# Optimization experiments

Measured on AMD Instinct MI355X. Metric: run time of the kernel, lower is better.

Reference implementation:

```python
import jax, jax.numpy as jnp
import numpy as np

B, S, D = 8, 4096, 1024
H = 16
HD = D // H          # 64
FF = 128             # FeedForward default intermediate_size
EPS = 1e-6           # flax RMSNorm default


def _rmsnorm(x, g):
    return x * jax.lax.rsqrt(jnp.mean(x * x, axis=-1, keepdims=True) + EPS) * g


def setup_inputs() -> dict:
    key = jax.random.key(0)
    ks = jax.random.split(key, 12)
    s = 0.02
    return {
        "x": jax.random.normal(ks[0], (B, S, D), jnp.float32),
        "attention_mask": jnp.ones((B, HD), jnp.int32),
        # per-head QKV projections stacked over heads: [H, D, HD]
        "Wq": jax.random.normal(ks[1], (H, D, HD), jnp.float32) * s,
        "bq": jnp.zeros((H, HD), jnp.float32),
        "Wk": jax.random.normal(ks[2], (H, D, HD), jnp.float32) * s,
        "bk": jnp.zeros((H, HD), jnp.float32),
        "Wv": jax.random.normal(ks[3], (H, D, HD), jnp.float32) * s,
        "bv": jnp.zeros((H, HD), jnp.float32),
        "Wo": jax.random.normal(ks[4], (D, D), jnp.float32) * s,
        "bo": jnp.zeros((D,), jnp.float32),
        "W1": jax.random.normal(ks[5], (D, FF), jnp.float32) * s,
        "b1": jnp.zeros((FF,), jnp.float32),
        "W2": jax.random.normal(ks[6], (FF, D), jnp.float32) * s,
        "b2": jnp.zeros((D,), jnp.float32),
        "g1": jnp.ones((D,), jnp.float32),
        "g2": jnp.ones((D,), jnp.float32),
    }


def reference(x, attention_mask, Wq, bq, Wk, bk, Wv, bv, Wo, bo, W1, b1, W2, b2, g1, g2):
    # per-head projections, vectorized over heads: [B, H, S, HD]
    q = jnp.einsum('bsd,hde->bhse', x, Wq) + bq[:, None, :]
    k = jnp.einsum('bsd,hde->bhse', x, Wk) + bk[:, None, :]
    v = jnp.einsum('bsd,hde->bhse', x, Wv) + bv[:, None, :]
    # scores = k^T @ q -> [B, H, HD(kfeat), HD(qfeat)]  (feature-feature attention)
    scores = jnp.einsum('bhsk,bhsq->bhkq', k, q)
    # tiled mask: each row of [HD, HD] equals mask -> masks along last (q-feature) axis
    m = attention_mask[:, None, None, :]  # [B,1,1,HD]
    scores = jnp.where(m == 0, -jnp.inf, scores)
    w = jax.nn.softmax(scores / jnp.sqrt(jnp.float32(HD)), axis=-2)
    # out = v @ w -> [B, H, S, HD]
    attn = jnp.einsum('bhsk,bhkq->bhsq', v, w)
    attn = attn.transpose(0, 2, 1, 3).reshape(B, S, D)  # concat heads
    # output projection + residual + RMSNorm
    h = x + attn @ Wo + bo
    h = _rmsnorm(h, g1)
    # tanh FFN + residual + RMSNorm
    ff = jnp.tanh(h @ W1 + b1) @ W2 + b2
    out = _rmsnorm(h + ff, g2)
    return out
```

## Files before the change

### kernel.cpp

```cpp
#include <hip/hip_runtime.h>
#include <math.h>

typedef __attribute__((ext_vector_type(4))) float f32x4;
typedef __attribute__((ext_vector_type(8))) short short8;
typedef __attribute__((ext_vector_type(4))) short short4v;

__device__ __forceinline__ float b2f(unsigned short u) {
  unsigned int x = ((unsigned int)u) << 16;
  return __builtin_bit_cast(float, x);
}
__device__ __forceinline__ unsigned short f2b(float f) {
  unsigned int x = __builtin_bit_cast(unsigned int, f);
  x += 0x7fffu + ((x >> 16) & 1u);
  return (unsigned short)(x >> 16);
}

__device__ __forceinline__ void gload16(const unsigned short* g, unsigned short* l) {
  __builtin_amdgcn_global_load_lds(
      (__attribute__((address_space(1))) void*)(unsigned long long)(const void*)g,
      (__attribute__((address_space(3))) void*)l, 16, 0, 0);
}

#define BARR  { __builtin_amdgcn_sched_barrier(0); __builtin_amdgcn_s_barrier(); __builtin_amdgcn_sched_barrier(0); }
#define LBARR { __builtin_amdgcn_sched_barrier(0); asm volatile("s_waitcnt lgkmcnt(0)" ::: "memory"); __builtin_amdgcn_s_barrier(); __builtin_amdgcn_sched_barrier(0); }
#define VMW(n) { __builtin_amdgcn_sched_barrier(0); asm volatile("s_waitcnt vmcnt(" #n ")" ::: "memory"); __builtin_amdgcn_sched_barrier(0); }

__global__ __launch_bounds__(256) void prep_kernel(
    const float* __restrict__ x, unsigned short* __restrict__ xb,
    const float* __restrict__ Wq, const float* __restrict__ Wk,
    const float* __restrict__ Wv, const float* __restrict__ Wo,
    const float* __restrict__ W1, const float* __restrict__ W2,
    const float* __restrict__ bq, const float* __restrict__ bk, const float* __restrict__ bv,
    const float* __restrict__ g1,
    unsigned short* __restrict__ BqkT, unsigned short* __restrict__ WoT,
    unsigned short* __restrict__ W1T, unsigned short* __restrict__ W2T,
    unsigned short* __restrict__ WvR,
    float* __restrict__ bqkv) {
  __shared__ float tile[64][65];
  int nb = blockIdx.x, t = threadIdx.x;
  if (nb < 16384) {
    long i = (long)nb * 256 + t;
    f32x4 a = ((const f32x4*)x)[i * 2];
    f32x4 b = ((const f32x4*)x)[i * 2 + 1];
    short8 o;
#pragma unroll
    for (int j = 0; j < 4; ++j) { o[j] = (short)f2b(a[j]); o[4 + j] = (short)f2b(b[j]); }
    ((short8*)xb)[i] = o;
    return;
  }
  int n0 = nb - 16384;
  if (n0 == 1088) {
#pragma unroll
    for (int it = 0; it < 12; ++it) {
      int idx = it * 256 + t;
      float v = (idx < 1024) ? bq[idx] : (idx < 2048 ? bk[idx - 1024] : bv[idx - 2048]);
      bqkv[idx] = v;
    }
    return;
  }
  if (n0 >= 832) {
    int rem = n0 - 832, h = rem >> 4, dc = rem & 15;
    int r = t >> 2, c0 = (t & 3) * 16;
    const float* s = Wv + ((long)h * 1024 + dc * 64 + r) * 64 + c0;
    unsigned short* d = WvR + (long)(dc * 64 + r) * 1024 + h * 64 + c0;
#pragma unroll
    for (int j4 = 0; j4 < 4; ++j4) {
      f32x4 v = *(const f32x4*)(s + j4 * 4);
      short4v o;
#pragma unroll
      for (int j = 0; j < 4; ++j) o[j] = (short)f2b(v[j]);
      *(short4v*)(d + j4 * 4) = o;
    }
    return;
  }
  const float* src; unsigned short* dst; int sld, dld;
  bool foldg = false; int dbase = 0;
  if (n0 < 512) {
    int w = n0 >> 8, rem = n0 & 255, h = rem >> 4, dc = rem & 15;
    const float* W = (w == 0) ? Wq : Wk;
    src = W + ((long)h * 1024 + dc * 64) * 64;                 sld = 64;
    dst = BqkT + (long)(w * 1024 + h * 64) * 1024 + dc * 64;   dld = 1024;
  } else if (n0 < 768) {
    int rem = n0 - 512, dr = rem >> 4, jc = rem & 15;
    src = Wo + (long)dr * 64 * 1024 + jc * 64;                 sld = 1024;
    dst = WoT + (long)jc * 64 * 1024 + dr * 64;                dld = 1024;
  } else if (n0 < 800) {
    int rem = n0 - 768, dr = rem >> 1, fc = rem & 1;
    src = W1 + (long)dr * 64 * 128 + fc * 64;                  sld = 128;
    dst = W1T + (long)fc * 64 * 1024 + dr * 64;                dld = 1024;
    foldg = true; dbase = dr * 64;
  } else {
    int rem = n0 - 800, fr = rem >> 4, jc = rem & 15;
    src = W2 + (long)fr * 64 * 1024 + jc * 64;                 sld = 1024;
    dst = W2T + (long)jc * 64 * 128 + fr * 64;                 dld = 128;
  }
  int r = t >> 2, c0 = (t & 3) * 16;
#pragma unroll
  for (int j4 = 0; j4 < 4; ++j4) {
    f32x4 v = *(const f32x4*)(src + (long)r * sld + c0 + j4 * 4);
    tile[c0 + j4 * 4 + 0][r] = v[0];
    tile[c0 + j4 * 4 + 1][r] = v[1];
    tile[c0 + j4 * 4 + 2][r] = v[2];
    tile[c0 + j4 * 4 + 3][r] = v[3];
  }
  __syncthreads();
  short8 o0, o1;
#pragma unroll
  for (int j = 0; j < 8; ++j) {
    float v0 = tile[r][c0 + j], v1 = tile[r][c0 + 8 + j];
    if (foldg) { v0 *= g1[dbase + c0 + j]; v1 *= g1[dbase + c0 + 8 + j]; }
    o0[j] = (short)f2b(v0);
    o1[j] = (short)f2b(v1);
  }
  *(short8*)(dst + (long)r * dld + c0) = o0;
  *(short8*)(dst + (long)r * dld + c0 + 8) = o1;
}

__device__ __forceinline__ void rdA2(short8 (&dst)[4][2], const char* paK0,
                                     const char* paK1, int off) {
#pragma unroll
  for (int fr = 0; fr < 4; ++fr) {
    dst[fr][0] = *(const short8*)(paK0 + off + fr * 2048);
    dst[fr][1] = *(const short8*)(paK1 + off + fr * 2048);
  }
}
__device__ __forceinline__ void rdB2(short8 (&dst)[2][2], const char* pbK0,
                                     const char* pbK1, int off) {
#pragma unroll
  for (int gr = 0; gr < 2; ++gr) {
    dst[gr][0] = *(const short8*)(pbK0 + off + gr * 2048);
    dst[gr][1] = *(const short8*)(pbK1 + off + gr * 2048);
  }
}
template <int BPH>
__device__ __forceinline__ void mfmaq_f(const short8 (&afr)[4][2], const short8 (&bf)[2][2],
                                        f32x4 (*ac)[4]) {
  __builtin_amdgcn_s_setprio(1);
#pragma unroll
  for (int fi = 0; fi < 4; ++fi)
#pragma unroll
    for (int gj = 0; gj < 2; ++gj)
#pragma unroll
      for (int ks = 0; ks < 2; ++ks)
        ac[fi][BPH * 2 + gj] = __builtin_amdgcn_mfma_f32_16x16x32_bf16(
            afr[fi][ks], bf[gj][ks], ac[fi][BPH * 2 + gj], 0, 0, 0);
  __builtin_amdgcn_s_setprio(0);
}

template <int EPI, int BSEL, int BBIAS>
__global__ __launch_bounds__(512, 2) void gemm8p(
    const unsigned short* __restrict__ A, int lda,
    const unsigned short* __restrict__ Bt, int ldb,
    unsigned short* __restrict__ C, int ldc,
    const float* __restrict__ bias,
    const unsigned short* __restrict__ residb, int ldr,
    float* __restrict__ ssb, const float* __restrict__ aux,
    int K, int NBX) {
  extern __shared__ char smb[];
  const int tid = threadIdx.x;
  const int lane = tid & 63, wid = tid >> 6;
  const int wm = wid >> 2, wn = wid & 3;

  int orig = blockIdx.x;
  int xcd = orig & 7, j = orig >> 3;
  int perx = gridDim.x >> 3;
  int mpx = perx / NBX;
  int ms = j / (4 * NBX), nb = (j >> 2) % NBX, mq = j & 3;
  const long m0 = (long)(xcd * mpx + ms * 4 + mq) * 256;
  const long n0 = (long)nb * 256;
  const unsigned short* bt = BSEL ? (Bt + (m0 >> 12) * 1048576) : Bt;
  const float* biasp = BBIAS ? (bias + (m0 >> 12) * 1024) : bias;

  const int NT = K >> 6, NI = NT >> 1;

  const int lr = lane & 15, lc = (lane >> 4) * 16;
  const int eA = lc ^ ((lr & 7) << 4);
  const char* paK0 = smb + wm * 8192 + lr * 128 + eA;
  const char* paK1 = smb + wm * 8192 + lr * 128 + (eA ^ 64);
  const char* pbK0 = smb + 65536 + wn * 4096 + lr * 128 + eA;
  const char* pbK1 = smb + 65536 + wn * 4096 + lr * 128 + (eA ^ 64);

  short8 afr0[4][2], afr1[4][2];
  short8 bfr0[2][2], bfr1[2][2];
  f32x4 acc[8][4] = {};

  auto stA = [&](int buf, int ph, int kt) {
#pragma unroll
    for (int rnd = 0; rnd < 2; ++rnd) {
      int o = rnd * 8192 + tid * 16;
      int wms = o >> 13, rsw = (o >> 7) & 63, cb = o & 127;
      int pcb = cb ^ ((rsw & 7) << 4);
      const unsigned short* src = A + (m0 + wms * 128 + ph * 64 + rsw) * (long)lda + kt * 64 + (pcb >> 1);
      gload16(src, (unsigned short*)(smb + buf * 32768 + ph * 16384 + o));
    }
  };
  auto stB = [&](int buf, int ph, int kt) {
#pragma unroll
    for (int rnd = 0; rnd < 2; ++rnd) {
      int o = rnd * 8192 + tid * 16;
      int wns = (o >> 12) & 3, rsw = (o >> 7) & 31, cb = o & 127;
      int pcb = cb ^ ((rsw & 7) << 4);
      const unsigned short* src = bt + (n0 + wns * 64 + ph * 32 + rsw) * (long)ldb + kt * 64 + (pcb >> 1);
      gload16(src, (unsigned short*)(smb + 65536 + buf * 32768 + ph * 16384 + o));
    }
  };

  stA(0, 0, 0); stA(0, 1, 0); stB(0, 0, 0); stB(0, 1, 0);
  stA(1, 0, 1); stA(1, 1, 1); stB(1, 0, 1); stB(1, 1, 1);
  VMW(8);
  BARR;
  rdA2(afr0, paK0, paK1, 0);
  rdB2(bfr0, pbK0, pbK1, 0);

  for (int i = 0; i < NI; ++i) {
    int t2 = 2 * i + 2, t3 = 2 * i + 3;
    bool more = t2 < NT;
    LBARR;
    rdB2(bfr1, pbK0, pbK1, 16384);
    mfmaq_f<0>(afr0, bfr0, &acc[0]);
    LBARR;
    rdA2(afr1, paK0, paK1, 16384);
    mfmaq_f<1>(afr0, bfr1, &acc[0]);
    LBARR;
    if (more) { stA(0, 0, t2); stA(0, 1, t2); }
    mfmaq_f<0>(afr1, bfr0, &acc[4]);
    if (more) { VMW(4); } else { VMW(0); }
    LBARR;
    rdA2(afr0, paK0, paK1, 32768);
    rdB2(bfr0, pbK0, pbK1, 32768);
    if (more) { stB(0, 0, t2); stB(0, 1, t2); }
    mfmaq_f<1>(afr1, bfr1, &acc[4]);
    LBARR;
    rdB2(bfr1, pbK0, pbK1, 32768 + 16384);
    mfmaq_f<0>(afr0, bfr0, &acc[0]);
    LBARR;
    rdA2(afr1, paK0, paK1, 32768 + 16384);
    mfmaq_f<1>(afr0, bfr1, &acc[0]);
    LBARR;
    if (more) { stA(1, 0, t3); stA(1, 1, t3); }
    mfmaq_f<0>(afr1, bfr0, &acc[4]);
    if (more) { VMW(4); } else { VMW(0); }
    LBARR;
    if (more) { rdA2(afr0, paK0, paK1, 0); rdB2(bfr0, pbK0, pbK1, 0); }
    if (more) { stB(1, 0, t3); stB(1, 1, t3); }
    mfmaq_f<1>(afr1, bfr1, &acc[4]);
  }

#pragma unroll
  for (int f = 0; f < 8; ++f) {
    float ssp[4] = {0.0f, 0.0f, 0.0f, 0.0f};
#pragma unroll
    for (int g = 0; g < 4; ++g) {
      long col = n0 + wn * 64 + g * 16 + (lane & 15);
      float bv = (EPI == 6) ? 0.0f : biasp[col];
      if (EPI == 7) bv += aux[col];
      float gv = (EPI == 5) ? aux[col] : 0.0f;
#pragma unroll
      for (int r = 0; r < 4; ++r) {
        long row = m0 + wm * 128 + f * 16 + (lane >> 4) * 4 + r;
        float o = acc[f][g][r] + bv;
        if (EPI == 7) o += b2f(residb[row * (long)ldr + col]);
        if (EPI == 5) {
          float rsv = rsqrtf(ssb[row] * (1.0f / 1024.0f) + 1e-6f);
          o += b2f(residb[row * (long)ldr + col]) * rsv * gv;
        }
        if (EPI == 7) ssp[r] += o * o;
        C[row * (long)ldc + col] = f2b(o);
      }
    }
    if (EPI == 7) {
#pragma unroll
      for (int r = 0; r < 4; ++r) {
        float p = ssp[r];
        p += __shfl_xor(p, 1, 64);
        p += __shfl_xor(p, 2, 64);
        p += __shfl_xor(p, 4, 64);
        p += __shfl_xor(p, 8, 64);
        if ((lane & 15) == 0) {
          long row = m0 + wm * 128 + f * 16 + (lane >> 4) * 4 + r;
          atomicAdd(&ssb[row], p);
        }
      }
    }
  }
}

template <int EPI>
__global__ __launch_bounds__(256, 2) void gemm_bt(
    const unsigned short* __restrict__ A, int lda,
    const unsigned short* __restrict__ Bt, int ldb,
    unsigned short* __restrict__ C, int ldc,
    const float* __restrict__ bias, const float* __restrict__ ssb, int K) {
  __shared__ __align__(16) unsigned short Asm[128 * 32];
  __shared__ __align__(16) unsigned short Bsm[128 * 32];
  const int tid = threadIdx.x;
  const int lane = tid & 63, wid = tid >> 6;
  const int wr = wid >> 1, wc = wid & 1;
  const long m0 = (long)blockIdx.y * 128;
  const long n0 = (long)blockIdx.x * 128;

  f32x4 acc[4][4] = {};

  for (int kk = 0; kk < K; kk += 32) {
    __syncthreads();
#pragma unroll
    for (int i = 0; i < 2; ++i) {
      int slot = i * 256 + tid;
      int r = slot >> 2, cg = (slot & 3) * 8;
      gload16(A + (m0 + r) * (long)lda + kk + cg, &Asm[slot * 8]);
      gload16(Bt + (n0 + r) * (long)ldb + kk + cg, &Bsm[slot * 8]);
    }
    __syncthreads();
    short8 af[4], bfr[4];
#pragma unroll
    for (int mt = 0; mt < 4; ++mt)
      af[mt] = *(const short8*)&Asm[(wr * 64 + mt * 16 + (lane & 15)) * 32 + (lane >> 4) * 8];
#pragma unroll
    for (int nt = 0; nt < 4; ++nt)
      bfr[nt] = *(const short8*)&Bsm[(wc * 64 + nt * 16 + (lane & 15)) * 32 + (lane >> 4) * 8];
#pragma unroll
    for (int mt = 0; mt < 4; ++mt)
#pragma unroll
      for (int nt = 0; nt < 4; ++nt)
        acc[mt][nt] = __builtin_amdgcn_mfma_f32_16x16x32_bf16(af[mt], bfr[nt], acc[mt][nt], 0, 0, 0);
  }

  const long row0 = m0 + wr * 64 + ((lane >> 4) * 4);
  const long col0 = n0 + wc * 64 + (lane & 15);
#pragma unroll
  for (int mt = 0; mt < 4; ++mt) {
#pragma unroll
    for (int nt = 0; nt < 4; ++nt) {
      long col = col0 + nt * 16;
      float bv = bias[col];
      f32x4 v = acc[mt][nt];
#pragma unroll
      for (int r = 0; r < 4; ++r) {
        long row = row0 + mt * 16 + r;
        float o = v[r];
        if (EPI == 4) {
          float rsv = rsqrtf(ssb[row] * (1.0f / 1024.0f) + 1e-6f);
          o = tanhf(o * rsv + bv);
        } else o += bv;
        C[row * (long)ldc + col] = f2b(o);
      }
    }
  }
}

__device__ __forceinline__ int sperm(int e) { return ((e + (e >> 3)) & 7) << 4; }

__global__ __launch_bounds__(256) void scores_mfma(
    const unsigned short* __restrict__ QK, float* __restrict__ part) {
  __shared__ __align__(16) char lds[32768];
  int bh = blockIdx.x, seg = blockIdx.y;
  int b = bh >> 4, h = bh & 15;
  int tid = threadIdx.x, lane = tid & 63, wid = tid >> 6;
  int e0 = (tid & 7) * 8;
  int sl0 = (tid >> 3) * 4;
  const unsigned short* Qg = QK + h * 64;
  const unsigned short* Kg = QK + 1024 + h * 64;
  f32x4 acc[4] = {};

  for (int ch = 0; ch < 8; ++ch) {
    long S0 = (long)b * 4096 + seg * 1024 + ch * 128;
    __syncthreads();
    short8 kv0 = *(const short8*)(Kg + (S0 + sl0 + 0) * 2048 + e0);
    short8 kv1 = *(const short8*)(Kg + (S0 + sl0 + 1) * 2048 + e0);
    short8 kv2 = *(const short8*)(Kg + (S0 + sl0 + 2) * 2048 + e0);
    short8 kv3 = *(const short8*)(Kg + (S0 + sl0 + 3) * 2048 + e0);
    short8 qv0 = *(const short8*)(Qg + (S0 + sl0 + 0) * 2048 + e0);
    short8 qv1 = *(const short8*)(Qg + (S0 + sl0 + 1) * 2048 + e0);
    short8 qv2 = *(const short8*)(Qg + (S0 + sl0 + 2) * 2048 + e0);
    short8 qv3 = *(const short8*)(Qg + (S0 + sl0 + 3) * 2048 + e0);
#pragma unroll
    for (int je = 0; je < 8; ++je) {
      int e = e0 + je;
      int sw = sperm(e);
      char* rowK = lds + e * 256;
      char* rowQ = lds + 16384 + e * 256;
      unsigned int klo = (unsigned short)kv0[je] | ((unsigned int)(unsigned short)kv1[je] << 16);
      unsigned int khi = (unsigned short)kv2[je] | ((unsigned int)(unsigned short)kv3[je] << 16);
      unsigned int qlo = (unsigned short)qv0[je] | ((unsigned int)(unsigned short)qv1[je] << 16);
      unsigned int qhi = (unsigned short)qv2[je] | ((unsigned int)(unsigned short)qv3[je] << 16);
      *(unsigned int*)(rowK + ((sl0 * 2) ^ sw)) = klo;
      *(unsigned int*)(rowK + ((sl0 * 2 + 4) ^ sw)) = khi;
      *(unsigned int*)(rowQ + ((sl0 * 2) ^ sw)) = qlo;
      *(unsigned int*)(rowQ + ((sl0 * 2 + 4) ^ sw)) = qhi;
    }
    __syncthreads();
#pragma unroll
    for (int ksi = 0; ksi < 4; ++ksi) {
      int colb = ksi * 64 + (lane >> 4) * 16;
      int erA = wid * 16 + (lane & 15);
      short8 af = *(const short8*)(lds + erA * 256 + (colb ^ sperm(erA)));
#pragma unroll
      for (int n = 0; n < 4; ++n) {
        int erB = n * 16 + (lane & 15);
        short8 bf = *(const short8*)(lds + 16384 + erB * 256 + (colb ^ sperm(erB)));
        acc[n] = __builtin_amdgcn_mfma_f32_16x16x32_bf16(af, bf, acc[n], 0, 0, 0);
      }
    }
  }
  float* dst = part + ((long)bh * 4 + seg) * 4096;
#pragma unroll
  for (int n = 0; n < 4; ++n)
#pragma unroll
    for (int r = 0; r < 4; ++r) {
      int k = wid * 16 + (lane >> 4) * 4 + r;
      int q = n * 16 + (lane & 15);
      dst[k * 64 + q] = acc[n][r];
    }
}

__global__ __launch_bounds__(64) void softmax_Wb(
    const float* __restrict__ part, const int* __restrict__ mask,
    unsigned short* __restrict__ Wb) {
  __shared__ float lt[64][65];
  int bh = blockIdx.x, q = threadIdx.x;
  int b = bh >> 4;
  const float* p0 = part + (long)bh * 4 * 4096;
  float s[64];
#pragma unroll
  for (int k = 0; k < 64; ++k)
    s[k] = p0[k * 64 + q] + p0[4096 + k * 64 + q] + p0[8192 + k * 64 + q] + p0[12288 + k * 64 + q];
  bool live = (mask[b * 64 + q] != 0);
  float m = -1e30f;
#pragma unroll
  for (int k = 0; k < 64; ++k) m = fmaxf(m, s[k]);
  float sum = 0.0f;
#pragma unroll
  for (int k = 0; k < 64; ++k) {
    s[k] = __expf((s[k] - m) * 0.125f);
    sum += s[k];
  }
  float inv = live ? 1.0f / sum : 0.0f;
#pragma unroll
  for (int k = 0; k < 64; ++k) lt[k][q] = s[k] * inv;
  __syncthreads();
  unsigned short* o = Wb + (long)bh * 4096 + q * 64;
#pragma unroll
  for (int j8 = 0; j8 < 8; ++j8) {
    short8 ov;
#pragma unroll
    for (int j = 0; j < 8; ++j) ov[j] = (short)f2b(lt[q][j8 * 8 + j]);
    *(short8*)(o + j8 * 8) = ov;
  }
}

__global__ __launch_bounds__(256) void wpt_kernel(
    const unsigned short* __restrict__ WoT, const unsigned short* __restrict__ Wb,
    unsigned short* __restrict__ WPT, const float* __restrict__ bv,
    float* __restrict__ hb) {
  int dblk = blockIdx.x;
  int h = blockIdx.y;
  int b = blockIdx.z;
  int tid = threadIdx.x, lane = tid & 63, wid = tid >> 6;
  int d0 = dblk * 256 + wid * 64;
  const unsigned short* wb = Wb + (long)(b * 16 + h) * 4096;
  f32x4 acc[4][4] = {};
#pragma unroll
  for (int ks = 0; ks < 2; ++ks) {
    short8 bf[4];
#pragma unroll
    for (int nt = 0; nt < 4; ++nt)
      bf[nt] = *(const short8*)(wb + (nt * 16 + (lane & 15)) * 64 + ks * 32 + (lane >> 4) * 8);
#pragma unroll
    for (int mt = 0; mt < 4; ++mt) {
      short8 af = *(const short8*)(WoT + (long)(d0 + mt * 16 + (lane & 15)) * 1024 + h * 64 + ks * 32 + (lane >> 4) * 8);
#pragma unroll
      for (int nt = 0; nt < 4; ++nt)
        acc[mt][nt] = __builtin_amdgcn_mfma_f32_16x16x32_bf16(af, bf[nt], acc[mt][nt], 0, 0, 0);
    }
  }
  float bvv[4];
#pragma unroll
  for (int nt = 0; nt < 4; ++nt) bvv[nt] = bv[h * 64 + nt * 16 + (lane & 15)];
#pragma unroll
  for (int mt = 0; mt < 4; ++mt) {
#pragma unroll
    for (int r = 0; r < 4; ++r) {
      long row = d0 + mt * 16 + (lane >> 4) * 4 + r;
      float p = 0.0f;
#pragma unroll
      for (int nt = 0; nt < 4; ++nt) {
        float o = acc[mt][nt][r];
        WPT[(long)b * 1048576 + row * 1024 + h * 64 + nt * 16 + (lane & 15)] = f2b(o);
        p += o * bvv[nt];
      }
      p += __shfl_xor(p, 1, 64);
      p += __shfl_xor(p, 2, 64);
      p += __shfl_xor(p, 4, 64);
      p += __shfl_xor(p, 8, 64);
      if ((lane & 15) == 0) atomicAdd(&hb[b * 1024 + row], p);
    }
  }
}

__global__ __launch_bounds__(256) void rmsnorm_k(
    const unsigned short* __restrict__ in, const float* __restrict__ g,
    float* __restrict__ outf) {
  long row = blockIdx.x;
  int tid = threadIdx.x;
  short4v u = *(const short4v*)(in + row * 1024 + tid * 4);
  float v[4];
  float ss = 0.0f;
#pragma unroll
  for (int i = 0; i < 4; ++i) {
    v[i] = b2f((unsigned short)u[i]);
    ss += v[i] * v[i];
  }
#pragma unroll
  for (int off = 32; off > 0; off >>= 1) ss += __shfl_xor(ss, off, 64);
  __shared__ float wsum[4];
  if ((tid & 63) == 0) wsum[tid >> 6] = ss;
  __syncthreads();
  float tot = wsum[0] + wsum[1] + wsum[2] + wsum[3];
  float rsv = rsqrtf(tot * (1.0f / 1024.0f) + 1e-6f);
  f32x4 gv = *(const f32x4*)(g + tid * 4);
  f32x4 ov;
#pragma unroll
  for (int i = 0; i < 4; ++i) ov[i] = v[i] * rsv * gv[i];
  *(f32x4*)(outf + row * 1024 + tid * 4) = ov;
}

extern "C" void kernel_launch(void* const* d_in, const int* in_sizes, int n_in,
                              void* d_out, int out_size, void* d_ws, size_t ws_size,
                              hipStream_t stream) {
  const float* x  = (const float*)d_in[0];
  const int* mask = (const int*)d_in[1];
  const float* Wq = (const float*)d_in[2];
  const float* bq = (const float*)d_in[3];
  const float* Wk = (const float*)d_in[4];
  const float* bk = (const float*)d_in[5];
  const float* Wv = (const float*)d_in[6];
  const float* bv = (const float*)d_in[7];
  const float* Wo = (const float*)d_in[8];
  const float* bo = (const float*)d_in[9];
  const float* W1 = (const float*)d_in[10];
  const float* b1 = (const float*)d_in[11];
  const float* W2 = (const float*)d_in[12];
  const float* b2 = (const float*)d_in[13];
  const float* g1 = (const float*)d_in[14];
  const float* g2 = (const float*)d_in[15];

  char* ws = (char*)d_ws;
  size_t off = 0;
  auto alc = [&](size_t n) { size_t o = off; off += (n + 255) & ~(size_t)255; return o; };
  unsigned short* BqkT  = (unsigned short*)(ws + alc(2048UL * 1024 * 2));
  unsigned short* WoT   = (unsigned short*)(ws + alc(1024UL * 1024 * 2));
  unsigned short* W1T   = (unsigned short*)(ws + alc(128UL * 1024 * 2));
  unsigned short* W2T   = (unsigned short*)(ws + alc(1024UL * 128 * 2));
  unsigned short* WvR   = (unsigned short*)(ws + alc(1024UL * 1024 * 2));
  float*          bqkv  = (float*)(ws + alc(3072UL * 4));
  float*          HBb   = (float*)(ws + alc(8192UL * 4));
  unsigned short* R0    = (unsigned short*)(ws + alc(32768UL * 1024 * 2));
  unsigned short* R1    = (unsigned short*)(ws + alc(32768UL * 2048 * 2));
  unsigned short* R2    = (unsigned short*)(ws + alc(32768UL * 1024 * 2));
  unsigned short* WPb   = (unsigned short*)(ws + alc(8UL * 1048576 * 2));
  unsigned short* WVPb  = (unsigned short*)(ws + alc(8UL * 1048576 * 2));
  unsigned short* Tb    = (unsigned short*)(ws + alc(32768UL * 128 * 2));
  float*          SP    = (float*)(ws + alc(512UL * 4096 * 4));
  unsigned short* Wbuf  = (unsigned short*)(ws + alc(128UL * 4096 * 2));
  float*          SSb   = (float*)(ws + alc(32768UL * 4));
  if (ws_size < off) return;

  unsigned short* xb   = R0;
  unsigned short* HFb  = R0;
  unsigned short* QKb  = R1;
  unsigned short* H1b  = R2;
  float* outp = (float*)d_out;

  hipMemsetAsync(HBb, 0, 8192 * 4, stream);
  hipMemsetAsync(SSb, 0, 32768 * 4, stream);
  prep_kernel<<<17473, 256, 0, stream>>>(x, xb, Wq, Wk, Wv, Wo, W1, W2, bq, bk, bv, g1,
                                         BqkT, WoT, W1T, W2T, WvR, bqkv);
  gemm8p<0, 0, 0><<<1024, 512, 131072, stream>>>(xb, 1024, BqkT, 1024, QKb, 2048,
                                                 bqkv, nullptr, 0, nullptr, nullptr,
                                                 1024, 8);
  scores_mfma<<<dim3(128, 4), 256, 0, stream>>>(QKb, SP);
  softmax_Wb<<<128, 64, 0, stream>>>(SP, mask, Wbuf);
  wpt_kernel<<<dim3(4, 16, 8), 256, 0, stream>>>(WoT, Wbuf, WPb, bqkv + 2048, HBb);
  gemm8p<6, 0, 0><<<128, 512, 131072, stream>>>(WPb, 1024, WvR, 1024, WVPb, 1024,
                                                nullptr, nullptr, 0, nullptr, nullptr,
                                                1024, 4);
  gemm8p<7, 1, 1><<<512, 512, 131072, stream>>>(xb, 1024, WVPb, 1024, H1b, 1024,
                                                HBb, xb, 1024, SSb, bo,
                                                1024, 4);
  gemm_bt<4><<<dim3(1, 256), 256, 0, stream>>>(H1b, 1024, W1T, 1024, Tb, 128, b1, SSb, 1024);
  gemm8p<5, 0, 0><<<512, 512, 131072, stream>>>(Tb, 128, W2T, 128, HFb, 1024,
                                                b2, H1b, 1024, SSb, g1,
                                                128, 4);
  rmsnorm_k<<<32768, 256, 0, stream>>>(HFb, g2, outp);
}
```

Before: 453.7 us.

## Replace 8-wave ping-pong GEMM with 16-wave single-phase K32 double-buffered GEMM

The 256x256-tile GEMM changes from 8 waves (512 threads) with an 8-phase ping-pong schedule over K=64 slices to 16 waves (1024 threads), each computing a 64x64 subtile over K=32 slices. A and B now share one swizzled 32 KB stage buffer, double-buffered in 64 KB of LDS instead of 128 KB. The aim is more waves to hide latency, less LDS, and simpler code. In exchange, each wave gets less register-level reuse, barriers come more often per unit of K, and the hand-tuned interleaving of LDS reads with MFMA is lost.

New measurement: 478.6 us. 1.05x slower.

```diff
diff --git a/kernel.cpp b/kernel.cpp
--- a/kernel.cpp
+++ b/kernel.cpp
@@ -116,39 +116,8 @@
   *(short8*)(dst + (long)r * dld + c0 + 8) = o1;
 }
 
-__device__ __forceinline__ void rdA2(short8 (&dst)[4][2], const char* paK0,
-                                     const char* paK1, int off) {
-#pragma unroll
-  for (int fr = 0; fr < 4; ++fr) {
-    dst[fr][0] = *(const short8*)(paK0 + off + fr * 2048);
-    dst[fr][1] = *(const short8*)(paK1 + off + fr * 2048);
-  }
-}
-__device__ __forceinline__ void rdB2(short8 (&dst)[2][2], const char* pbK0,
-                                     const char* pbK1, int off) {
-#pragma unroll
-  for (int gr = 0; gr < 2; ++gr) {
-    dst[gr][0] = *(const short8*)(pbK0 + off + gr * 2048);
-    dst[gr][1] = *(const short8*)(pbK1 + off + gr * 2048);
-  }
-}
-template <int BPH>
-__device__ __forceinline__ void mfmaq_f(const short8 (&afr)[4][2], const short8 (&bf)[2][2],
-                                        f32x4 (*ac)[4]) {
-  __builtin_amdgcn_s_setprio(1);
-#pragma unroll
-  for (int fi = 0; fi < 4; ++fi)
-#pragma unroll
-    for (int gj = 0; gj < 2; ++gj)
-#pragma unroll
-      for (int ks = 0; ks < 2; ++ks)
-        ac[fi][BPH * 2 + gj] = __builtin_amdgcn_mfma_f32_16x16x32_bf16(
-            afr[fi][ks], bf[gj][ks], ac[fi][BPH * 2 + gj], 0, 0, 0);
-  __builtin_amdgcn_s_setprio(0);
-}
-
 template <int EPI, int BSEL, int BBIAS>
-__global__ __launch_bounds__(512, 2) void gemm8p(
+__global__ __launch_bounds__(1024, 4) void gemm16w(
     const unsigned short* __restrict__ A, int lda,
     const unsigned short* __restrict__ Bt, int ldb,
     unsigned short* __restrict__ C, int ldc,
@@ -171,83 +140,56 @@
   const unsigned short* bt = BSEL ? (Bt + (m0 >> 12) * 1048576) : Bt;
   const float* biasp = BBIAS ? (bias + (m0 >> 12) * 1024) : bias;
 
-  const int NT = K >> 6, NI = NT >> 1;
-
-  const int lr = lane & 15, lc = (lane >> 4) * 16;
-  const int eA = lc ^ ((lr & 7) << 4);
-  const char* paK0 = smb + wm * 8192 + lr * 128 + eA;
-  const char* paK1 = smb + wm * 8192 + lr * 128 + (eA ^ 64);
-  const char* pbK0 = smb + 65536 + wn * 4096 + lr * 128 + eA;
-  const char* pbK1 = smb + 65536 + wn * 4096 + lr * 128 + (eA ^ 64);
-
-  short8 afr0[4][2], afr1[4][2];
-  short8 bfr0[2][2], bfr1[2][2];
-  f32x4 acc[8][4] = {};
-
-  auto stA = [&](int buf, int ph, int kt) {
-#pragma unroll
-    for (int rnd = 0; rnd < 2; ++rnd) {
-      int o = rnd * 8192 + tid * 16;
-      int wms = o >> 13, rsw = (o >> 7) & 63, cb = o & 127;
-      int pcb = cb ^ ((rsw & 7) << 4);
-      const unsigned short* src = A + (m0 + wms * 128 + ph * 64 + rsw) * (long)lda + kt * 64 + (pcb >> 1);
-      gload16(src, (unsigned short*)(smb + buf * 32768 + ph * 16384 + o));
-    }
+  const int NT = K >> 5;
+
+  const int lr = lane & 15, lg = lane >> 4;
+  const char* pA = smb + wm * 8192 + lr * 128 + ((lg ^ (lr & 7)) << 4);
+  const char* pB = smb + wn * 8192 + lr * 128 + (((4 + lg) ^ (lr & 7)) << 4);
+
+  f32x4 acc[4][4] = {};
+
+  auto stage = [&](int buf, int half, int kt) {
+    int o = half * 16384 + tid * 16;
+    int r = o >> 7, sl = (o >> 4) & 7;
+    int v = sl ^ (r & 7);
+    const unsigned short* src = (v < 4)
+        ? A + (m0 + r) * (long)lda + kt * 32 + v * 8
+        : bt + (n0 + r) * (long)ldb + kt * 32 + (v - 4) * 8;
+    gload16(src, (unsigned short*)(smb + buf + o));
   };
-  auto stB = [&](int buf, int ph, int kt) {
-#pragma unroll
-    for (int rnd = 0; rnd < 2; ++rnd) {
-      int o = rnd * 8192 + tid * 16;
-      int wns = (o >> 12) & 3, rsw = (o >> 7) & 31, cb = o & 127;
-      int pcb = cb ^ ((rsw & 7) << 4);
-      const unsigned short* src = bt + (n0 + wns * 64 + ph * 32 + rsw) * (long)ldb + kt * 64 + (pcb >> 1);
-      gload16(src, (unsigned short*)(smb + 65536 + buf * 32768 + ph * 16384 + o));
-    }
-  };
-
-  stA(0, 0, 0); stA(0, 1, 0); stB(0, 0, 0); stB(0, 1, 0);
-  stA(1, 0, 1); stA(1, 1, 1); stB(1, 0, 1); stB(1, 1, 1);
-  VMW(8);
+
+  stage(0, 0, 0); stage(0, 1, 0);
+  stage(32768, 0, 1); stage(32768, 1, 1);
+  VMW(2);
   BARR;
-  rdA2(afr0, paK0, paK1, 0);
-  rdB2(bfr0, pbK0, pbK1, 0);
-
-  for (int i = 0; i < NI; ++i) {
-    int t2 = 2 * i + 2, t3 = 2 * i + 3;
-    bool more = t2 < NT;
+
+  for (int t = 0; t < NT; ++t) {
+    int buf = (t & 1) << 15;
+    short8 afr[4], bfr[4];
+#pragma unroll
+    for (int f = 0; f < 4; ++f) afr[f] = *(const short8*)(pA + buf + f * 2048);
+#pragma unroll
+    for (int g = 0; g < 4; ++g) bfr[g] = *(const short8*)(pB + buf + g * 2048);
+    __builtin_amdgcn_s_setprio(1);
+#pragma unroll
+    for (int f = 0; f < 4; ++f)
+#pragma unroll
+      for (int g = 0; g < 4; ++g)
+        acc[f][g] = __builtin_amdgcn_mfma_f32_16x16x32_bf16(afr[f], bfr[g], acc[f][g], 0, 0, 0);
+    __builtin_amdgcn_s_setprio(0);
     LBARR;
-    rdB2(bfr1, pbK0, pbK1, 16384);
-    mfmaq_f<0>(afr0, bfr0, &acc[0]);
-    LBARR;
-    rdA2(afr1, paK0, paK1, 16384);
-    mfmaq_f<1>(afr0, bfr1, &acc[0]);
-    LBARR;
-    if (more) { stA(0, 0, t2); stA(0, 1, t2); }
-    mfmaq_f<0>(afr1, bfr0, &acc[4]);
-    if (more) { VMW(4); } else { VMW(0); }
-    LBARR;
-    rdA2(afr0, paK0, paK1, 32768);
-    rdB2(bfr0, pbK0, pbK1, 32768);
-    if (more) { stB(0, 0, t2); stB(0, 1, t2); }
-    mfmaq_f<1>(afr1, bfr1, &acc[4]);
-    LBARR;
-    rdB2(bfr1, pbK0, pbK1, 32768 + 16384);
-    mfmaq_f<0>(afr0, bfr0, &acc[0]);
-    LBARR;
-    rdA2(afr1, paK0, paK1, 32768 + 16384);
-    mfmaq_f<1>(afr0, bfr1, &acc[0]);
-    LBARR;
-    if (more) { stA(1, 0, t3); stA(1, 1, t3); }
-    mfmaq_f<0>(afr1, bfr0, &acc[4]);
-    if (more) { VMW(4); } else { VMW(0); }
-    LBARR;
-    if (more) { rdA2(afr0, paK0, paK1, 0); rdB2(bfr0, pbK0, pbK1, 0); }
-    if (more) { stB(1, 0, t3); stB(1, 1, t3); }
-    mfmaq_f<1>(afr1, bfr1, &acc[4]);
-  }
-
-#pragma unroll
-  for (int f = 0; f < 8; ++f) {
+    if (t + 2 < NT) {
+      stage(buf, 0, t + 2);
+      stage(buf, 1, t + 2);
+      VMW(2);
+    } else {
+      VMW(0);
+    }
+    BARR;
+  }
+
+#pragma unroll
+  for (int f = 0; f < 4; ++f) {
     float ssp[4] = {0.0f, 0.0f, 0.0f, 0.0f};
 #pragma unroll
     for (int g = 0; g < 4; ++g) {
@@ -257,7 +199,7 @@
       float gv = (EPI == 5) ? aux[col] : 0.0f;
 #pragma unroll
       for (int r = 0; r < 4; ++r) {
-        long row = m0 + wm * 128 + f * 16 + (lane >> 4) * 4 + r;
+        long row = m0 + wm * 64 + f * 16 + (lane >> 4) * 4 + r;
         float o = acc[f][g][r] + bv;
         if (EPI == 7) o += b2f(residb[row * (long)ldr + col]);
         if (EPI == 5) {
@@ -277,7 +219,7 @@
         p += __shfl_xor(p, 4, 64);
         p += __shfl_xor(p, 8, 64);
         if ((lane & 15) == 0) {
-          long row = m0 + wm * 128 + f * 16 + (lane >> 4) * 4 + r;
+          long row = m0 + wm * 64 + f * 16 + (lane >> 4) * 4 + r;
           atomicAdd(&ssb[row], p);
         }
       }
@@ -575,21 +517,21 @@
   hipMemsetAsync(SSb, 0, 32768 * 4, stream);
   prep_kernel<<<17473, 256, 0, stream>>>(x, xb, Wq, Wk, Wv, Wo, W1, W2, bq, bk, bv, g1,
                                          BqkT, WoT, W1T, W2T, WvR, bqkv);
-  gemm8p<0, 0, 0><<<1024, 512, 131072, stream>>>(xb, 1024, BqkT, 1024, QKb, 2048,
-                                                 bqkv, nullptr, 0, nullptr, nullptr,
-                                                 1024, 8);
+  gemm16w<0, 0, 0><<<1024, 1024, 65536, stream>>>(xb, 1024, BqkT, 1024, QKb, 2048,
+                                                  bqkv, nullptr, 0, nullptr, nullptr,
+                                                  1024, 8);
   scores_mfma<<<dim3(128, 4), 256, 0, stream>>>(QKb, SP);
   softmax_Wb<<<128, 64, 0, stream>>>(SP, mask, Wbuf);
   wpt_kernel<<<dim3(4, 16, 8), 256, 0, stream>>>(WoT, Wbuf, WPb, bqkv + 2048, HBb);
-  gemm8p<6, 0, 0><<<128, 512, 131072, stream>>>(WPb, 1024, WvR, 1024, WVPb, 1024,
-                                                nullptr, nullptr, 0, nullptr, nullptr,
-                                                1024, 4);
-  gemm8p<7, 1, 1><<<512, 512, 131072, stream>>>(xb, 1024, WVPb, 1024, H1b, 1024,
-                                                HBb, xb, 1024, SSb, bo,
-                                                1024, 4);
+  gemm16w<6, 0, 0><<<128, 1024, 65536, stream>>>(WPb, 1024, WvR, 1024, WVPb, 1024,
+                                                 nullptr, nullptr, 0, nullptr, nullptr,
+                                                 1024, 4);
+  gemm16w<7, 1, 1><<<512, 1024, 65536, stream>>>(xb, 1024, WVPb, 1024, H1b, 1024,
+                                                 HBb, xb, 1024, SSb, bo,
+                                                 1024, 4);
   gemm_bt<4><<<dim3(1, 256), 256, 0, stream>>>(H1b, 1024, W1T, 1024, Tb, 128, b1, SSb, 1024);
-  gemm8p<5, 0, 0><<<512, 512, 131072, stream>>>(Tb, 128, W2T, 128, HFb, 1024,
-                                                b2, H1b, 1024, SSb, g1,
-                                                128, 4);
+  gemm16w<5, 0, 0><<<512, 1024, 65536, stream>>>(Tb, 128, W2T, 128, HFb, 1024,
+                                                 b2, H1b, 1024, SSb, g1,
+                                                 128, 4);
   rmsnorm_k<<<32768, 256, 0, stream>>>(HFb, g2, outp);
 }
```
